# Optimization experiments

Hardware: AMD Instinct MI355X
Metric: run time of the kernel (lower is better)

## Reference

```python
import jax, jax.numpy as jnp
import numpy as np

B, S, D, H, E, HID = 4, 1024, 768, 12, 8, 3072
DH = D // H

def _ln(x, g, b, eps=1e-5):
    m = jnp.mean(x, -1, keepdims=True)
    v = jnp.mean((x - m) ** 2, -1, keepdims=True)
    return (x - m) * jax.lax.rsqrt(v + eps) * g + b

def setup_inputs():
    key = jax.random.key(0)
    ks = jax.random.split(key, 16)
    p = lambda k, s: jax.random.normal(k, s, jnp.float32) * 0.02
    causal = jnp.triu(jnp.ones((S, S), bool), 1)  # True = masked (future)
    return {
        "x": jax.random.normal(ks[0], (B, S, D), jnp.float32),
        "mask": jnp.broadcast_to(causal, (B, S, S)),
        "ln_attn_g": jnp.ones((D,), jnp.float32), "ln_attn_b": jnp.zeros((D,), jnp.float32),
        "wq": p(ks[1], (D, D)), "bq": jnp.zeros((D,), jnp.float32),
        "wk": p(ks[2], (D, D)), "bk": jnp.zeros((D,), jnp.float32),
        "wv": p(ks[3], (D, D)), "bv": jnp.zeros((D,), jnp.float32),
        "wo": p(ks[4], (D, D)), "bo": jnp.zeros((D,), jnp.float32),
        "ln_ff_g": jnp.ones((D,), jnp.float32), "ln_ff_b": jnp.zeros((D,), jnp.float32),
        "gate_w": p(ks[5], (D, E)), "gate_b": jnp.zeros((E,), jnp.float32),
        "w1": p(ks[6], (E, D, HID)), "b1": jnp.zeros((E, HID), jnp.float32),
        "w2": p(ks[7], (E, HID, D)), "b2": jnp.zeros((E, D), jnp.float32),
        "moe_ln_g": jnp.ones((D,), jnp.float32), "moe_ln_b": jnp.zeros((D,), jnp.float32),
        "top_k": 2,
    }

def reference(x, mask, ln_attn_g, ln_attn_b, wq, bq, wk, bk, wv, bv, wo, bo,
              ln_ff_g, ln_ff_b, gate_w, gate_b, w1, b1, w2, b2,
              moe_ln_g, moe_ln_b, top_k):
    # --- pre-LN multi-head self-attention + residual ---
    a = _ln(x, ln_attn_g, ln_attn_b)
    q = (a @ wq + bq).reshape(B, S, H, DH)
    k = (a @ wk + bk).reshape(B, S, H, DH)
    v = (a @ wv + bv).reshape(B, S, H, DH)
    scores = jnp.einsum("bqhd,bkhd->bhqk", q, k) / jnp.sqrt(jnp.float32(DH))
    scores = jnp.where(mask[:, None, :, :], jnp.float32(-1e9), scores)
    probs = jax.nn.softmax(scores, axis=-1)
    ctx = jnp.einsum("bhqk,bkhd->bqhd", probs, v).reshape(B, S, D)
    x = x + (ctx @ wo + bo)
    # --- MoE positionwise FF (CustomizedMoEPositionwiseFF, pre_lnorm=False) ---
    h = _ln(x, ln_ff_g, ln_ff_b)                        # ln_ff(x) fed into ff
    logits = h @ gate_w + gate_b                        # [B,S,E] naive gate
    vals, idx = jax.lax.top_k(logits, top_k)            # [B,S,k]
    sc = jax.nn.softmax(vals, axis=-1)                  # softmax over top-k logits
    # dense all-expert compute (dropless reference for dispatch+grouped GEMM)
    e1 = jax.nn.relu(jnp.einsum("bsd,edh->bseh", h, w1) + b1)  # [B,S,E,HID]
    e2 = jnp.einsum("bseh,ehd->bsed", e1, w2) + b2             # [B,S,E,D]
    sel = jnp.take_along_axis(e2, idx[..., None], axis=2)      # [B,S,k,D]
    core = jnp.sum(sel * sc[..., None], axis=2)                # combine
    moe_out = _ln(h + core, moe_ln_g, moe_ln_b)                # post-lnorm
    return x + moe_out
```

## Files before the change

### kernel.cpp

```cpp
#include <hip/hip_runtime.h>
#include <hip/hip_bf16.h>
#include <stdint.h>

using bf16 = __hip_bfloat16;
typedef short s16x8 __attribute__((ext_vector_type(8)));
typedef float f32x4 __attribute__((ext_vector_type(4)));

#define NB 4
#define NS 1024
#define ND 768
#define NH 12
#define NE 8
#define NHID 3072
#define NTOK 4096
#define NASSIGN 8192
#define MAXCH 72
#define MAXSLOT (MAXCH * 128)

__device__ __forceinline__ float bf2f(bf16 v){ return __bfloat162float(v); }
__device__ __forceinline__ bf16 f2bf(float v){ return __float2bfloat16(v); }

__device__ __forceinline__ void gload_lds16(const bf16* g, bf16* l){
  __builtin_amdgcn_global_load_lds((const __attribute__((address_space(1))) void*)g,
                                   (__attribute__((address_space(3))) void*)l, 16, 0, 0);
}

__device__ __forceinline__ void transpose64_body(const float* __restrict__ src,
                                                 bf16* __restrict__ dst,
                                                 int K, int N, int n0, int k0, int t){
  __shared__ float tile[64][65];
  int kr = t >> 4, c4 = (t & 15) * 4;
  #pragma unroll
  for (int i = 0; i < 4; i++){
    int k = kr + i * 16;
    float4 v = *(const float4*)(src + (size_t)(k0 + k) * N + n0 + c4);
    tile[k][c4]     = v.x;
    tile[k][c4 + 1] = v.y;
    tile[k][c4 + 2] = v.z;
    tile[k][c4 + 3] = v.w;
  }
  __syncthreads();
  int nr = t >> 3, k8 = (t & 7) * 8;
  #pragma unroll
  for (int i = 0; i < 2; i++){
    int n = nr + i * 32;
    short vv[8];
    #pragma unroll
    for (int j = 0; j < 8; j++){
      bf16 x = f2bf(tile[k8 + j][n]);
      vv[j] = *(short*)&x;
    }
    *(s16x8*)(dst + (size_t)(n0 + n) * K + k0 + k8) = *(s16x8*)vv;
  }
}

__global__ void transpose_convert_kernel(const float* __restrict__ src, bf16* __restrict__ dst,
                                         int K, int N){
  int bz = blockIdx.z;
  transpose64_body(src + (size_t)bz * K * N, dst + (size_t)bz * N * K,
                   K, N, blockIdx.x * 64, blockIdx.y * 64, threadIdx.x);
}

struct Ptr4 { const float* p0; const float* p1; const float* p2; const float* p3; };
__global__ void transpose4_kernel(Ptr4 s4, bf16* __restrict__ dst){
  int z = blockIdx.z;
  const float* src = (z == 0) ? s4.p0 : (z == 1) ? s4.p1 : (z == 2) ? s4.p2 : s4.p3;
  transpose64_body(src, dst + (size_t)z * 768 * 768,
                   768, 768, blockIdx.x * 64, blockIdx.y * 64, threadIdx.x);
}

__global__ void concat3_kernel(const float* __restrict__ a, const float* __restrict__ b,
                               const float* __restrict__ c, float* __restrict__ out){
  int i = blockIdx.x * 256 + threadIdx.x;
  if (i >= 3 * ND) return;
  float v = (i < ND) ? a[i] : (i < 2 * ND ? b[i - ND] : c[i - 2 * ND]);
  out[i] = v;
}

template<bool OF, bool OB>
__global__ void ln_kernel(const float* __restrict__ in, const float* __restrict__ g,
                          const float* __restrict__ bb, float* __restrict__ of,
                          bf16* __restrict__ ob){
  int row = blockIdx.x, t = threadIdx.x;
  const float* x = in + (size_t)row * ND;
  float v[3]; float s = 0.f, sq = 0.f;
  #pragma unroll
  for (int i = 0; i < 3; i++){ v[i] = x[t + i * 256]; s += v[i]; sq += v[i] * v[i]; }
  __shared__ float rs[4], rq[4];
  #pragma unroll
  for (int d = 32; d >= 1; d >>= 1){ s += __shfl_xor(s, d); sq += __shfl_xor(sq, d); }
  int w = t >> 6;
  if ((t & 63) == 0){ rs[w] = s; rq[w] = sq; }
  __syncthreads();
  s = rs[0] + rs[1] + rs[2] + rs[3];
  sq = rq[0] + rq[1] + rq[2] + rq[3];
  float mean = s * (1.f / ND);
  float var = sq * (1.f / ND) - mean * mean;
  float rstd = rsqrtf(var + 1e-5f);
  #pragma unroll
  for (int i = 0; i < 3; i++){
    int idx = t + i * 256;
    float y = (v[i] - mean) * rstd * g[idx] + bb[idx];
    if (OF) of[(size_t)row * ND + idx] = y;
    if (OB) ob[(size_t)row * ND + idx] = f2bf(y);
  }
}

template<int GROUP, bool GATHER, bool RELU, bool OBF, bool RESID, bool SEG>
__global__ __launch_bounds__(256, 3)
void gemm_kernel(const bf16* __restrict__ A, int ldA,
                 const bf16* __restrict__ BtB,
                 const float* __restrict__ biasB,
                 void* __restrict__ Cv, int ldC,
                 const float* __restrict__ resid,
                 int N, int K,
                 const int* __restrict__ chunk_e, const int* __restrict__ tok){
  __shared__ __align__(16) bf16 sA[2][128 * 32];
  __shared__ __align__(16) bf16 sB[2][128 * 32];

  int t = threadIdx.x;
  int lane = t & 63, wv = t >> 6;
  int c0i = wv * 128 + lane;
  int r0  = c0i >> 2;
  int kk  = (c0i & 3) * 8;
  int nt = blockIdx.x;
  int wm = (wv >> 1) * 64, wn = (wv & 1) * 64;
  int l16 = lane & 15, q4 = lane >> 4;
  int aoff[4], boff[4];
  #pragma unroll
  for (int mi = 0; mi < 4; mi++) aoff[mi] = (wm + mi * 16 + l16) * 32 + q4 * 8;
  #pragma unroll
  for (int ni = 0; ni < 4; ni++) boff[ni] = (wn + ni * 16 + l16) * 32 + q4 * 8;

  for (int g = 0; g < GROUP; g++){
    int c = blockIdx.y * GROUP + g;
    int e = 0;
    if (SEG){ e = chunk_e[c]; if (e < 0) break; }
    const bf16* Bt = SEG ? BtB + (size_t)e * N * K : BtB;
    const float* bias = SEG ? biasB + (size_t)e * N : biasB;
    size_t arow0, arow1;
    int m0 = c * 128 + r0, m1 = m0 + 16;
    if (GATHER){ arow0 = (size_t)tok[m0]; arow1 = (size_t)tok[m1]; }
    else       { arow0 = (size_t)m0;      arow1 = (size_t)m1; }
    const bf16* gA0 = A + arow0 * ldA + kk;
    const bf16* gA1 = A + arow1 * ldA + kk;
    const bf16* gB0 = Bt + (size_t)(nt * 128 + r0) * K + kk;
    const bf16* gB1 = Bt + (size_t)(nt * 128 + r0 + 16) * K + kk;

    if (g > 0) __syncthreads();

    f32x4 acc[4][4] = {};
    gload_lds16(gA0, &sA[0][(size_t)c0i * 8]);
    gload_lds16(gA1, &sA[0][(size_t)(c0i + 64) * 8]);
    gload_lds16(gB0, &sB[0][(size_t)c0i * 8]);
    gload_lds16(gB1, &sB[0][(size_t)(c0i + 64) * 8]);

    int nk = K >> 5;
    for (int ki = 0; ki < nk; ki++){
      int cur = ki & 1;
      __syncthreads();
      if (ki + 1 < nk){
        int nxt = cur ^ 1, off = (ki + 1) * 32;
        gload_lds16(gA0 + off, &sA[nxt][(size_t)c0i * 8]);
        gload_lds16(gA1 + off, &sA[nxt][(size_t)(c0i + 64) * 8]);
        gload_lds16(gB0 + off, &sB[nxt][(size_t)c0i * 8]);
        gload_lds16(gB1 + off, &sB[nxt][(size_t)(c0i + 64) * 8]);
      }
      s16x8 af[4], bfr[4];
      #pragma unroll
      for (int mi = 0; mi < 4; mi++) af[mi] = *(const s16x8*)(&sA[cur][0] + aoff[mi]);
      #pragma unroll
      for (int ni = 0; ni < 4; ni++) bfr[ni] = *(const s16x8*)(&sB[cur][0] + boff[ni]);
      #pragma unroll
      for (int mi = 0; mi < 4; mi++)
        #pragma unroll
        for (int ni = 0; ni < 4; ni++)
          acc[mi][ni] = __builtin_amdgcn_mfma_f32_16x16x32_bf16(af[mi], bfr[ni], acc[mi][ni], 0, 0, 0);
    }

    #pragma unroll
    for (int mi = 0; mi < 4; mi++){
      #pragma unroll
      for (int ni = 0; ni < 4; ni++){
        int col = nt * 128 + wn + ni * 16 + l16;
        float bv = bias[col];
        #pragma unroll
        for (int r = 0; r < 4; r++){
          size_t crow = (size_t)(c * 128 + wm + mi * 16 + q4 * 4 + r);
          float v = acc[mi][ni][r] + bv;
          if (RELU) v = fmaxf(v, 0.f);
          if (RESID) v += resid[crow * ldC + col];
          if (OBF) ((bf16*)Cv)[crow * ldC + col] = f2bf(v);
          else     ((float*)Cv)[crow * ldC + col] = v;
        }
      }
    }
  }
}

__global__ void vtrans_kernel(const bf16* __restrict__ qkv, bf16* __restrict__ vT){
  __shared__ bf16 tile[64][65];
  int bh = blockIdx.z; int b = bh / NH, h = bh % NH;
  int s0 = blockIdx.x * 64;
  int t = threadIdx.x;
  int sr = t >> 3, d8 = (t & 7) * 8;
  #pragma unroll
  for (int i = 0; i < 2; i++){
    int s = sr + i * 32;
    s16x8 v = *(const s16x8*)(qkv + (size_t)(b * NS + s0 + s) * 2304 + 1536 + h * 64 + d8);
    #pragma unroll
    for (int j = 0; j < 8; j++) tile[d8 + j][s] = ((bf16*)&v)[j];
  }
  __syncthreads();
  int dr = t >> 3, s8 = (t & 7) * 8;
  #pragma unroll
  for (int i = 0; i < 2; i++){
    int d = dr + i * 32;
    short vv[8];
    #pragma unroll
    for (int j = 0; j < 8; j++){ bf16 x = tile[d][s8 + j]; vv[j] = *(short*)&x; }
    *(s16x8*)(vT + ((size_t)bh * 64 + d) * NS + s0 + s8) = *(s16x8*)vv;
  }
}

#define SPAD 72
__global__ __launch_bounds__(256, 3)
void flash_attn_kernel(const bf16* __restrict__ qkv, const bf16* __restrict__ vT,
                       bf16* __restrict__ ctx){
  __shared__ __align__(16) bf16 sK[2][64 * 64];
  __shared__ __align__(16) bf16 sV[2][64 * 64];
  __shared__ __align__(16) bf16 sP[4][16 * SPAD];
  int id = blockIdx.x;
  int bh = id % 48;
  int qt = 15 - (id / 48);
  int b = bh / NH, h = bh % NH;
  int t = threadIdx.x, lane = t & 63, wv = t >> 6;
  int l16 = lane & 15, q4 = lane >> 4;
  int q0 = qt * 64 + wv * 16;
  const size_t ldq = 2304;
  const bf16* qbase = qkv + (size_t)(b * NS) * ldq + h * 64;
  const bf16* kbase = qbase + 768;
  const bf16* vtb = vT + (size_t)bh * 64 * NS;
  bf16* sPw = &sP[wv][0];
  const f32x4 fzero = {0.f, 0.f, 0.f, 0.f};

  s16x8 qf[2];
  #pragma unroll
  for (int kh = 0; kh < 2; kh++)
    qf[kh] = *(const s16x8*)(qbase + (size_t)(q0 + l16) * ldq + kh * 32 + q4 * 8);

  f32x4 O[4] = {};
  float ms[4], ls[4];
  #pragma unroll
  for (int r = 0; r < 4; r++){ ms[r] = -1e30f; ls[r] = 0.f; }

  int sub = lane >> 3, rawc = lane & 7;
  auto stage = [&](int buf, int key0){
    #pragma unroll
    for (int i = 0; i < 2; i++){
      int rk = wv * 8 + sub + i * 32;
      int cs = (rawc ^ (rk & 7)) * 8;
      gload_lds16(kbase + (size_t)(key0 + rk) * ldq + cs, &sK[buf][wv * 512 + i * 2048]);
      gload_lds16(vtb + (size_t)rk * NS + key0 + cs,      &sV[buf][wv * 512 + i * 2048]);
    }
  };

  int ntiles = qt + 1;
  stage(0, 0);
  for (int ti = 0; ti < ntiles; ti++){
    int cur = ti & 1, key0 = ti * 64;
    __syncthreads();
    if (ti + 1 < ntiles) stage(cur ^ 1, (ti + 1) * 64);
    if (key0 <= q0 + 15){
      const bf16* sKc = &sK[cur][0];
      const bf16* sVc = &sV[cur][0];
      s16x8 kf[4][2], vf[4][2];
      #pragma unroll
      for (int ni = 0; ni < 4; ni++){
        int krow = ni * 16 + l16;
        #pragma unroll
        for (int kh = 0; kh < 2; kh++)
          kf[ni][kh] = *(const s16x8*)(sKc + krow * 64 + (((kh * 4 + q4) ^ (krow & 7)) * 8));
      }
      #pragma unroll
      for (int dt = 0; dt < 4; dt++){
        int vrow = dt * 16 + l16;
        #pragma unroll
        for (int kh = 0; kh < 2; kh++)
          vf[dt][kh] = *(const s16x8*)(sVc + vrow * 64 + (((kh * 4 + q4) ^ (vrow & 7)) * 8));
      }
      f32x4 Sf[4];
      #pragma unroll
      for (int ni = 0; ni < 4; ni++){
        Sf[ni] = __builtin_amdgcn_mfma_f32_16x16x32_bf16(qf[0], kf[ni][0], fzero, 0, 0, 0);
        Sf[ni] = __builtin_amdgcn_mfma_f32_16x16x32_bf16(qf[1], kf[ni][1], Sf[ni], 0, 0, 0);
      }
      bool need_mask = (key0 + 63 >= q0);
      #pragma unroll
      for (int r = 0; r < 4; r++){
        int qrow = q0 + q4 * 4 + r;
        float sv[4];
        #pragma unroll
        for (int ni = 0; ni < 4; ni++){
          sv[ni] = Sf[ni][r] * 0.125f;
          if (need_mask && (key0 + ni * 16 + l16 > qrow)) sv[ni] = -1e30f;
        }
        float mx = fmaxf(fmaxf(sv[0], sv[1]), fmaxf(sv[2], sv[3]));
        #pragma unroll
        for (int d = 8; d >= 1; d >>= 1) mx = fmaxf(mx, __shfl_xor(mx, d));
        float mnew = fmaxf(ms[r], mx);
        float alpha = __expf(ms[r] - mnew);
        float p[4], psum = 0.f;
        #pragma unroll
        for (int ni = 0; ni < 4; ni++){ p[ni] = __expf(sv[ni] - mnew); psum += p[ni]; }
        #pragma unroll
        for (int d = 8; d >= 1; d >>= 1) psum += __shfl_xor(psum, d);
        ls[r] = ls[r] * alpha + psum;
        ms[r] = mnew;
        #pragma unroll
        for (int dt = 0; dt < 4; dt++) O[dt][r] *= alpha;
        int prow = q4 * 4 + r;
        #pragma unroll
        for (int ni = 0; ni < 4; ni++)
          sPw[prow * SPAD + ni * 16 + l16] = f2bf(p[ni]);
      }
      s16x8 pf[2];
      #pragma unroll
      for (int kh = 0; kh < 2; kh++)
        pf[kh] = *(const s16x8*)(sPw + l16 * SPAD + kh * 32 + q4 * 8);
      #pragma unroll
      for (int dt = 0; dt < 4; dt++){
        O[dt] = __builtin_amdgcn_mfma_f32_16x16x32_bf16(pf[0], vf[dt][0], O[dt], 0, 0, 0);
        O[dt] = __builtin_amdgcn_mfma_f32_16x16x32_bf16(pf[1], vf[dt][1], O[dt], 0, 0, 0);
      }
    }
  }

  #pragma unroll
  for (int r = 0; r < 4; r++){
    float inv = 1.f / ls[r];
    int qrow = q0 + q4 * 4 + r;
    #pragma unroll
    for (int dt = 0; dt < 4; dt++)
      ctx[(size_t)(b * NS + qrow) * ND + h * 64 + dt * 16 + l16] = f2bf(O[dt][r] * inv);
  }
}

__global__ __launch_bounds__(256)
void gate_kernel(const float* __restrict__ h, const float* __restrict__ gw,
                 const float* __restrict__ gb, int* __restrict__ ridx,
                 float* __restrict__ rw, int* __restrict__ counts){
  __shared__ float sgw[NE * ND];
  __shared__ int scnt[NE];
  int t = threadIdx.x;
  if (t < NE) scnt[t] = 0;
  for (int idx = t; idx < ND * NE; idx += 256){
    int i = idx >> 3, e = idx & 7;
    sgw[e * ND + i] = gw[idx];
  }
  __syncthreads();
  int lane = t & 63, wv = t >> 6;
  for (int it = 0; it < 8; it++){
    int tok = blockIdx.x * 32 + it * 4 + wv;
    const float* hr = h + (size_t)tok * ND;
    float acc[NE] = {};
    #pragma unroll
    for (int ii = 0; ii < 12; ii++){
      int i = lane + ii * 64;
      float hv = hr[i];
      #pragma unroll
      for (int e = 0; e < NE; e++) acc[e] += hv * sgw[e * ND + i];
    }
    #pragma unroll
    for (int e = 0; e < NE; e++)
      #pragma unroll
      for (int d = 32; d >= 1; d >>= 1) acc[e] += __shfl_xor(acc[e], d);
    if (lane == 0){
      float v0 = -1e30f, v1 = -1e30f; int i0 = 0, i1 = 0;
      #pragma unroll
      for (int e = 0; e < NE; e++){
        float v = acc[e] + gb[e];
        if (v > v0){ v1 = v0; i1 = i0; v0 = v; i0 = e; }
        else if (v > v1){ v1 = v; i1 = e; }
      }
      float w0 = 1.f / (1.f + __expf(v1 - v0));
      ridx[tok * 2] = i0; ridx[tok * 2 + 1] = i1;
      rw[tok * 2] = w0;  rw[tok * 2 + 1] = 1.f - w0;
      atomicAdd(&scnt[i0], 1);
      atomicAdd(&scnt[i1], 1);
    }
  }
  __syncthreads();
  if (t < NE) atomicAdd(&counts[t], scnt[t]);
}

__global__ void scan_kernel(const int* __restrict__ counts, int* __restrict__ poff,
                            int* __restrict__ chunk_e, int* __restrict__ tok_list){
  int t = threadIdx.x;
  for (int i = t; i < MAXSLOT; i += 256) tok_list[i] = 0;
  if (t == 0){
    int s = 0, c = 0;
    for (int e = 0; e < NE; e++){
      poff[e] = s;
      int nch = (counts[e] + 127) >> 7;
      for (int i = 0; i < nch; i++) chunk_e[c++] = e;
      s += nch << 7;
    }
    for (; c < MAXCH; c++) chunk_e[c] = -1;
  }
}

__global__ void scatter_kernel(const int* __restrict__ ridx, const int* __restrict__ poff,
                               int* __restrict__ cursor, int* __restrict__ tok_list,
                               int* __restrict__ slot_of){
  int tk = blockIdx.x * 256 + threadIdx.x;
  int lane = threadIdx.x & 63;
  int e = ridx[tk];
  unsigned long long lmask = (1ull << lane) - 1;
  int slot = 0;
  #pragma unroll
  for (int ee = 0; ee < NE; ee++){
    unsigned long long mask = __ballot(e == ee);
    if (mask == 0ull) continue;
    int leader = __ffsll((unsigned long long)mask) - 1;
    int base = 0;
    if (lane == leader) base = atomicAdd(&cursor[ee], __popcll(mask));
    base = __shfl(base, leader);
    if (e == ee) slot = poff[ee] + base + __popcll(mask & lmask);
  }
  tok_list[slot] = tk >> 1;
  slot_of[tk] = slot;
}

__global__ void combine_kernel(const bf16* __restrict__ e2, const int* __restrict__ slot_of,
                               const float* __restrict__ rw, const float* __restrict__ hf,
                               const float* __restrict__ attn_x, const float* __restrict__ g,
                               const float* __restrict__ bb, float* __restrict__ out){
  int row = blockIdx.x, t = threadIdx.x;
  int sl0 = slot_of[row * 2], sl1 = slot_of[row * 2 + 1];
  float w0 = rw[row * 2], w1 = rw[row * 2 + 1];
  const bf16* r0 = e2 + (size_t)sl0 * ND;
  const bf16* r1 = e2 + (size_t)sl1 * ND;
  const float* hr = hf + (size_t)row * ND;
  float v[3]; float s = 0.f, sq = 0.f;
  #pragma unroll
  for (int i = 0; i < 3; i++){
    int idx = t + i * 256;
    float c = w0 * bf2f(r0[idx]) + w1 * bf2f(r1[idx]);
    float xv = hr[idx] + c;
    v[i] = xv; s += xv; sq += xv * xv;
  }
  __shared__ float rs[4], rq[4];
  #pragma unroll
  for (int d = 32; d >= 1; d >>= 1){ s += __shfl_xor(s, d); sq += __shfl_xor(sq, d); }
  int w = t >> 6;
  if ((t & 63) == 0){ rs[w] = s; rq[w] = sq; }
  __syncthreads();
  s = rs[0] + rs[1] + rs[2] + rs[3];
  sq = rq[0] + rq[1] + rq[2] + rq[3];
  float mean = s * (1.f / ND);
  float var = sq * (1.f / ND) - mean * mean;
  float rstd = rsqrtf(var + 1e-5f);
  #pragma unroll
  for (int i = 0; i < 3; i++){
    int idx = t + i * 256;
    float y = (v[i] - mean) * rstd * g[idx] + bb[idx];
    out[(size_t)row * ND + idx] = attn_x[(size_t)row * ND + idx] + y;
  }
}

extern "C" void kernel_launch(void* const* d_in, const int* in_sizes, int n_in,
                              void* d_out, int out_size, void* d_ws, size_t ws_size,
                              hipStream_t stream){
  const float* x        = (const float*)d_in[0];
  const float* ln_att_g = (const float*)d_in[2];
  const float* ln_att_b = (const float*)d_in[3];
  const float* wq = (const float*)d_in[4];  const float* bq = (const float*)d_in[5];
  const float* wk = (const float*)d_in[6];  const float* bk = (const float*)d_in[7];
  const float* wv = (const float*)d_in[8];  const float* bv = (const float*)d_in[9];
  const float* wo = (const float*)d_in[10]; const float* bo = (const float*)d_in[11];
  const float* ln_ff_g = (const float*)d_in[12];
  const float* ln_ff_b = (const float*)d_in[13];
  const float* gate_w  = (const float*)d_in[14];
  const float* gate_b  = (const float*)d_in[15];
  const float* w1 = (const float*)d_in[16]; const float* b1 = (const float*)d_in[17];
  const float* w2 = (const float*)d_in[18]; const float* b2 = (const float*)d_in[19];
  const float* moe_g = (const float*)d_in[20];
  const float* moe_b = (const float*)d_in[21];

  uint8_t* p = (uint8_t*)d_ws;
  auto alloc = [&](size_t bytes) -> void* {
    void* r = (void*)p;
    p += (bytes + 255) & ~(size_t)255;
    return r;
  };
  bf16* wqkv_t  = (bf16*)alloc((size_t)(2304 + 768) * 768 * 2);
  bf16* wo_t    = wqkv_t + (size_t)2304 * 768;
  bf16* w1_t    = (bf16*)alloc((size_t)NE * NHID * ND * 2);
  bf16* w2_t    = (bf16*)alloc((size_t)NE * ND * NHID * 2);
  float* bias_qkv = (float*)alloc(2304 * 4);
  bf16* a_bf    = (bf16*)alloc((size_t)NTOK * ND * 2);
  bf16* qkv     = (bf16*)alloc((size_t)NTOK * 2304 * 2);
  bf16* vT      = (bf16*)alloc((size_t)NB * NH * 64 * NS * 2);
  bf16* ctx     = (bf16*)alloc((size_t)NTOK * ND * 2);
  float* attn_x = (float*)alloc((size_t)NTOK * ND * 4);
  float* h_f    = (float*)alloc((size_t)NTOK * ND * 4);
  bf16* h_b     = (bf16*)alloc((size_t)NTOK * ND * 2);
  int*  ridx    = (int*)alloc(NASSIGN * 4);
  float* rwt    = (float*)alloc(NASSIGN * 4);
  int* counts   = (int*)alloc(NE * 4);
  int* poff     = (int*)alloc(NE * 4);
  int* cursor   = (int*)alloc(NE * 4);
  int* chunk_e  = (int*)alloc(MAXCH * 4);
  int* tok_list = (int*)alloc(MAXSLOT * 4);
  int* slot_of  = (int*)alloc(NASSIGN * 4);
  bf16* e1      = (bf16*)alloc((size_t)MAXSLOT * NHID * 2);
  bf16* e2      = (bf16*)alloc((size_t)MAXSLOT * ND * 2);

  hipMemsetAsync(counts, 0, NE * 4, stream);
  hipMemsetAsync(cursor, 0, NE * 4, stream);

  Ptr4 s4; s4.p0 = wq; s4.p1 = wk; s4.p2 = wv; s4.p3 = wo;
  transpose4_kernel<<<dim3(12, 12, 4), 256, 0, stream>>>(s4, wqkv_t);
  transpose_convert_kernel<<<dim3(48, 12, NE), 256, 0, stream>>>(w1, w1_t, 768, 3072);
  transpose_convert_kernel<<<dim3(12, 48, NE), 256, 0, stream>>>(w2, w2_t, 3072, 768);
  concat3_kernel<<<dim3(9), 256, 0, stream>>>(bq, bk, bv, bias_qkv);

  ln_kernel<false, true><<<dim3(NTOK), 256, 0, stream>>>(x, ln_att_g, ln_att_b, nullptr, a_bf);
  gemm_kernel<2, false, false, true, false, false><<<dim3(18, 16), 256, 0, stream>>>(
      a_bf, ND, wqkv_t, bias_qkv, qkv, 2304, nullptr, 2304, ND, nullptr, nullptr);
  vtrans_kernel<<<dim3(16, 1, NB * NH), 256, 0, stream>>>(qkv, vT);
  flash_attn_kernel<<<dim3(768), 256, 0, stream>>>(qkv, vT, ctx);
  gemm_kernel<1, false, false, false, true, false><<<dim3(6, 32), 256, 0, stream>>>(
      ctx, ND, wo_t, bo, attn_x, ND, x, ND, ND, nullptr, nullptr);

  ln_kernel<true, true><<<dim3(NTOK), 256, 0, stream>>>(attn_x, ln_ff_g, ln_ff_b, h_f, h_b);
  gate_kernel<<<dim3(NTOK / 32), 256, 0, stream>>>(h_f, gate_w, gate_b, ridx, rwt, counts);
  scan_kernel<<<dim3(1), 256, 0, stream>>>(counts, poff, chunk_e, tok_list);
  scatter_kernel<<<dim3(NASSIGN / 256), 256, 0, stream>>>(ridx, poff, cursor, tok_list, slot_of);
  gemm_kernel<2, true, true, true, false, true><<<dim3(24, 36), 256, 0, stream>>>(
      h_b, ND, w1_t, b1, e1, NHID, nullptr, NHID, ND, chunk_e, tok_list);
  gemm_kernel<1, false, false, true, false, true><<<dim3(6, 72), 256, 0, stream>>>(
      e1, NHID, w2_t, b2, e2, ND, nullptr, ND, NHID, chunk_e, nullptr);
  combine_kernel<<<dim3(NTOK), 256, 0, stream>>>(e2, slot_of, rwt, h_f, attn_x, moe_g, moe_b,
                                                 (float*)d_out);
}
```

Before: 540.2 us.

## Split-K the second expert GEMM into two fp32 partials with XCD-aware block mapping

The down-projection expert GEMM (K=3072) is split into two K halves. Each half writes an fp32 partial buffer, and the combine kernel sums the two partials. Blocks are remapped so that blocks sharing a chunk land on the same XCD, which doubles the block count to 864 and improves occupancy and L2 locality. The QKV GEMM also moves from GROUP=2 to GROUP=1 with twice the grid rows. The cost is extra fp32 partial traffic and twice the combine reads, and empty chunks break early, which the combine never reads anyway.

```diff
diff --git a/kernel.cpp b/kernel.cpp
--- a/kernel.cpp
+++ b/kernel.cpp
@@ -106,14 +106,14 @@
   }
 }
 
-template<int GROUP, bool GATHER, bool RELU, bool OBF, bool RESID, bool SEG>
+template<int GROUP, bool GATHER, bool RELU, bool OBF, bool RESID, bool SEG, bool SPLITZ>
 __global__ __launch_bounds__(256, 3)
 void gemm_kernel(const bf16* __restrict__ A, int ldA,
                  const bf16* __restrict__ BtB,
                  const float* __restrict__ biasB,
                  void* __restrict__ Cv, int ldC,
                  const float* __restrict__ resid,
-                 int N, int K,
+                 int N, int K, int ldB, size_t czstride,
                  const int* __restrict__ chunk_e, const int* __restrict__ tok){
   __shared__ __align__(16) bf16 sA[2][128 * 32];
   __shared__ __align__(16) bf16 sB[2][128 * 32];
@@ -123,7 +123,18 @@
   int c0i = wv * 128 + lane;
   int r0  = c0i >> 2;
   int kk  = (c0i & 3) * 8;
-  int nt = blockIdx.x;
+  int nt, cbase = 0, ks = 0;
+  if (SPLITZ){
+    int l = blockIdx.x, xcd = l & 7, slot = l >> 3;
+    int grp = xcd + 8 * (slot / 6);
+    nt = slot % 6;
+    cbase = grp % MAXCH;
+    ks = grp / MAXCH;
+  } else {
+    nt = blockIdx.x;
+  }
+  int koff = ks * K;
+  float* Cfs = (float*)Cv + (size_t)ks * czstride;
   int wm = (wv >> 1) * 64, wn = (wv & 1) * 64;
   int l16 = lane & 15, q4 = lane >> 4;
   int aoff[4], boff[4];
@@ -133,19 +144,19 @@
   for (int ni = 0; ni < 4; ni++) boff[ni] = (wn + ni * 16 + l16) * 32 + q4 * 8;
 
   for (int g = 0; g < GROUP; g++){
-    int c = blockIdx.y * GROUP + g;
+    int c = SPLITZ ? cbase : blockIdx.y * GROUP + g;
     int e = 0;
     if (SEG){ e = chunk_e[c]; if (e < 0) break; }
-    const bf16* Bt = SEG ? BtB + (size_t)e * N * K : BtB;
+    const bf16* Bt = SEG ? BtB + (size_t)e * N * ldB : BtB;
     const float* bias = SEG ? biasB + (size_t)e * N : biasB;
     size_t arow0, arow1;
     int m0 = c * 128 + r0, m1 = m0 + 16;
     if (GATHER){ arow0 = (size_t)tok[m0]; arow1 = (size_t)tok[m1]; }
     else       { arow0 = (size_t)m0;      arow1 = (size_t)m1; }
-    const bf16* gA0 = A + arow0 * ldA + kk;
-    const bf16* gA1 = A + arow1 * ldA + kk;
-    const bf16* gB0 = Bt + (size_t)(nt * 128 + r0) * K + kk;
-    const bf16* gB1 = Bt + (size_t)(nt * 128 + r0 + 16) * K + kk;
+    const bf16* gA0 = A + arow0 * ldA + koff + kk;
+    const bf16* gA1 = A + arow1 * ldA + koff + kk;
+    const bf16* gB0 = Bt + (size_t)(nt * 128 + r0) * ldB + koff + kk;
+    const bf16* gB1 = Bt + (size_t)(nt * 128 + r0 + 16) * ldB + koff + kk;
 
     if (g > 0) __syncthreads();
 
@@ -183,7 +194,7 @@
       #pragma unroll
       for (int ni = 0; ni < 4; ni++){
         int col = nt * 128 + wn + ni * 16 + l16;
-        float bv = bias[col];
+        float bv = (!SPLITZ || ks == 0) ? bias[col] : 0.f;
         #pragma unroll
         for (int r = 0; r < 4; r++){
           size_t crow = (size_t)(c * 128 + wm + mi * 16 + q4 * 4 + r);
@@ -191,7 +202,7 @@
           if (RELU) v = fmaxf(v, 0.f);
           if (RESID) v += resid[crow * ldC + col];
           if (OBF) ((bf16*)Cv)[crow * ldC + col] = f2bf(v);
-          else     ((float*)Cv)[crow * ldC + col] = v;
+          else     Cfs[crow * ldC + col] = v;
         }
       }
     }
@@ -432,21 +443,23 @@
   slot_of[tk] = slot;
 }
 
-__global__ void combine_kernel(const bf16* __restrict__ e2, const int* __restrict__ slot_of,
+__global__ void combine_kernel(const float* __restrict__ e2p, const int* __restrict__ slot_of,
                                const float* __restrict__ rw, const float* __restrict__ hf,
                                const float* __restrict__ attn_x, const float* __restrict__ g,
                                const float* __restrict__ bb, float* __restrict__ out){
   int row = blockIdx.x, t = threadIdx.x;
   int sl0 = slot_of[row * 2], sl1 = slot_of[row * 2 + 1];
   float w0 = rw[row * 2], w1 = rw[row * 2 + 1];
-  const bf16* r0 = e2 + (size_t)sl0 * ND;
-  const bf16* r1 = e2 + (size_t)sl1 * ND;
+  const float* r0a = e2p + (size_t)sl0 * ND;
+  const float* r0b = r0a + (size_t)MAXSLOT * ND;
+  const float* r1a = e2p + (size_t)sl1 * ND;
+  const float* r1b = r1a + (size_t)MAXSLOT * ND;
   const float* hr = hf + (size_t)row * ND;
   float v[3]; float s = 0.f, sq = 0.f;
   #pragma unroll
   for (int i = 0; i < 3; i++){
     int idx = t + i * 256;
-    float c = w0 * bf2f(r0[idx]) + w1 * bf2f(r1[idx]);
+    float c = w0 * (r0a[idx] + r0b[idx]) + w1 * (r1a[idx] + r1b[idx]);
     float xv = hr[idx] + c;
     v[i] = xv; s += xv; sq += xv * xv;
   }
@@ -515,7 +528,7 @@
   int* tok_list = (int*)alloc(MAXSLOT * 4);
   int* slot_of  = (int*)alloc(NASSIGN * 4);
   bf16* e1      = (bf16*)alloc((size_t)MAXSLOT * NHID * 2);
-  bf16* e2      = (bf16*)alloc((size_t)MAXSLOT * ND * 2);
+  float* e2p    = (float*)alloc((size_t)2 * MAXSLOT * ND * 4);
 
   hipMemsetAsync(counts, 0, NE * 4, stream);
   hipMemsetAsync(cursor, 0, NE * 4, stream);
@@ -527,21 +540,22 @@
   concat3_kernel<<<dim3(9), 256, 0, stream>>>(bq, bk, bv, bias_qkv);
 
   ln_kernel<false, true><<<dim3(NTOK), 256, 0, stream>>>(x, ln_att_g, ln_att_b, nullptr, a_bf);
-  gemm_kernel<2, false, false, true, false, false><<<dim3(18, 16), 256, 0, stream>>>(
-      a_bf, ND, wqkv_t, bias_qkv, qkv, 2304, nullptr, 2304, ND, nullptr, nullptr);
+  gemm_kernel<1, false, false, true, false, false, false><<<dim3(18, 32), 256, 0, stream>>>(
+      a_bf, ND, wqkv_t, bias_qkv, qkv, 2304, nullptr, 2304, ND, ND, 0, nullptr, nullptr);
   vtrans_kernel<<<dim3(16, 1, NB * NH), 256, 0, stream>>>(qkv, vT);
   flash_attn_kernel<<<dim3(768), 256, 0, stream>>>(qkv, vT, ctx);
-  gemm_kernel<1, false, false, false, true, false><<<dim3(6, 32), 256, 0, stream>>>(
-      ctx, ND, wo_t, bo, attn_x, ND, x, ND, ND, nullptr, nullptr);
+  gemm_kernel<1, false, false, false, true, false, false><<<dim3(6, 32), 256, 0, stream>>>(
+      ctx, ND, wo_t, bo, attn_x, ND, x, ND, ND, ND, 0, nullptr, nullptr);
 
   ln_kernel<true, true><<<dim3(NTOK), 256, 0, stream>>>(attn_x, ln_ff_g, ln_ff_b, h_f, h_b);
   gate_kernel<<<dim3(NTOK / 32), 256, 0, stream>>>(h_f, gate_w, gate_b, ridx, rwt, counts);
   scan_kernel<<<dim3(1), 256, 0, stream>>>(counts, poff, chunk_e, tok_list);
   scatter_kernel<<<dim3(NASSIGN / 256), 256, 0, stream>>>(ridx, poff, cursor, tok_list, slot_of);
-  gemm_kernel<2, true, true, true, false, true><<<dim3(24, 36), 256, 0, stream>>>(
-      h_b, ND, w1_t, b1, e1, NHID, nullptr, NHID, ND, chunk_e, tok_list);
-  gemm_kernel<1, false, false, true, false, true><<<dim3(6, 72), 256, 0, stream>>>(
-      e1, NHID, w2_t, b2, e2, ND, nullptr, ND, NHID, chunk_e, nullptr);
-  combine_kernel<<<dim3(NTOK), 256, 0, stream>>>(e2, slot_of, rwt, h_f, attn_x, moe_g, moe_b,
+  gemm_kernel<2, true, true, true, false, true, false><<<dim3(24, 36), 256, 0, stream>>>(
+      h_b, ND, w1_t, b1, e1, NHID, nullptr, NHID, ND, ND, 0, chunk_e, tok_list);
+  gemm_kernel<1, false, false, false, false, true, true><<<dim3(864), 256, 0, stream>>>(
+      e1, NHID, w2_t, b2, e2p, ND, nullptr, ND, NHID / 2, NHID,
+      (size_t)MAXSLOT * ND, chunk_e, nullptr);
+  combine_kernel<<<dim3(NTOK), 256, 0, stream>>>(e2p, slot_of, rwt, h_f, attn_x, moe_g, moe_b,
                                                  (float*)d_out);
 }
```

Result: no change. 540.1 us (-0.0%).
